# Performance work log

Hardware: AMD Instinct MI355X
Metric: run time of the kernel (lower is better)

Reference implementation:

```python
import jax, jax.numpy as jnp
import numpy as np
from jax import lax

V = 33      # n_vertices
EPS = 1e-5  # instance-norm eps


def _resize_bilinear(x, oh, ow):
    # torch F.interpolate bilinear, align_corners=False, antialias=False
    b, c, H, W = x.shape
    def coords(out, size):
        src = (jnp.arange(out, dtype=jnp.float32) + 0.5) * (size / out) - 0.5
        i0 = jnp.clip(jnp.floor(src).astype(jnp.int32), 0, size - 1)
        i1 = jnp.clip(i0 + 1, 0, size - 1)
        f = jnp.clip(src - i0.astype(jnp.float32), 0.0, 1.0)
        return i0, i1, f
    y0, y1, fy = coords(oh, H)
    x0, x1, fx = coords(ow, W)
    rows = x[:, :, y0, :] * (1 - fy)[None, None, :, None] + x[:, :, y1, :] * fy[None, None, :, None]
    return rows[:, :, :, x0] * (1 - fx) + rows[:, :, :, x1] * fx


def _conv_s2(x, w, b):
    y = lax.conv_general_dilated(x, w, (2, 2), [(1, 1), (1, 1)],
                                 dimension_numbers=('NCHW', 'OIHW', 'NCHW'))
    return y + b[None, :, None, None]


def _lrelu(x):
    return jnp.where(x >= 0, x, 0.2 * x)


def _inorm(x, g, be):
    m = x.mean((2, 3), keepdims=True)
    v = x.var((2, 3), keepdims=True)
    return (x - m) / jnp.sqrt(v + EPS) * g[None, :, None, None] + be[None, :, None, None]


def _ailut_transform(imgs, luts, vertices):
    # imgs (b,3,H,W); luts (b,3,V,V,V) indexed [out_c, ib, ig, ir]; vertices (b,3,V)
    b, c, H, W = imgs.shape
    N = H * W
    x = jnp.clip(imgs, 0.0, 1.0).reshape(b, 3, N)
    ss = jax.vmap(jax.vmap(lambda v, q: jnp.searchsorted(v, q, side='right')))
    idx = jnp.clip(ss(vertices, x) - 1, 0, V - 2)            # (b,3,N)
    v0 = jnp.take_along_axis(vertices, idx, axis=-1)
    v1 = jnp.take_along_axis(vertices, idx + 1, axis=-1)
    frac = jnp.clip((x - v0) / jnp.maximum(v1 - v0, 1e-10), 0.0, 1.0)
    ir, ig, ibl = idx[:, 0], idx[:, 1], idx[:, 2]            # (b,N) each
    fr, fg, fb = frac[:, 0], frac[:, 1], frac[:, 2]
    lut_flat = luts.reshape(b, 3, V * V * V)
    out = jnp.zeros((b, 3, N), imgs.dtype)
    for db in (0, 1):
        wb = fb if db else 1.0 - fb
        for dg in (0, 1):
            wg = fg if dg else 1.0 - fg
            for dr in (0, 1):
                w = wb * wg * (fr if dr else 1.0 - fr)       # (b,N)
                flat = ((ibl + db) * V + (ig + dg)) * V + (ir + dr)
                vals = jnp.take_along_axis(lut_flat, jnp.broadcast_to(flat[:, None, :], (b, 3, N)), axis=-1)
                out = out + w[:, None, :] * vals
    return out.reshape(b, 3, H, W)


def setup_inputs() -> dict:
    key = jax.random.key(0)
    ks = jax.random.split(key, 32)
    n = lambda k, s: jax.random.normal(k, s, jnp.float32) * 0.05
    inp = {'imgs': jax.random.uniform(ks[0], (2, 3, 2048, 2048), jnp.float32)}
    chans = [(3, 16), (16, 32), (32, 64), (64, 128), (128, 128)]
    for i, (ci, co) in enumerate(chans, start=1):
        inp[f'w{i}'] = n(ks[2 * i], (co, ci, 3, 3))
        inp[f'b{i}'] = n(ks[2 * i + 1], (co,))
        if i <= 4:
            inp[f'g{i}'] = jnp.ones((co,), jnp.float32)
            inp[f'be{i}'] = jnp.zeros((co,), jnp.float32)
    inp['wgen_w'] = n(ks[12], (512, 3))
    inp['wgen_b'] = n(ks[13], (3,))
    inp['basis_w'] = n(ks[14], (3, 3 * V ** 3))
    inp['ada_w'] = n(ks[15], (512, 3 * (V - 1)))
    inp['ada_b'] = n(ks[16], (3 * (V - 1),))
    return inp


def reference(imgs, w1, b1, g1, be1, w2, b2, g2, be2, w3, b3, g3, be3,
              w4, b4, g4, be4, w5, b5, wgen_w, wgen_b, basis_w, ada_w, ada_b):
    b = imgs.shape[0]
    x = _resize_bilinear(imgs, 256, 256)
    for (w, bb, g, be) in ((w1, b1, g1, be1), (w2, b2, g2, be2),
                           (w3, b3, g3, be3), (w4, b4, g4, be4)):
        x = _inorm(_lrelu(_conv_s2(x, w, bb)), g, be)
    x = _lrelu(_conv_s2(x, w5, b5))                      # (b,128,8,8); dropout is identity at eval
    x = x.reshape(b, 128, 2, 4, 2, 4).mean((3, 5)).reshape(b, 512)  # AdaptiveAvgPool2d(2)
    weights = x @ wgen_w + wgen_b                        # (b,3) rank weights
    luts = (weights @ basis_w).reshape(b, 3, V, V, V)
    intervals = jax.nn.softmax((x @ ada_w + ada_b).reshape(b, 3, V - 1), axis=-1)
    vertices = jnp.pad(jnp.cumsum(intervals, -1), ((0, 0), (0, 0), (1, 0)))  # (b,3,V)
    return _ailut_transform(imgs, luts, vertices)
```

## Files before the change

kernel.cpp:

```cpp
#include <hip/hip_runtime.h>
#include <hip/hip_fp16.h>
#include <cstdint>
#include <cstddef>

#define VCUBE 35937
#define LUT_CH 107811

typedef float fx4 __attribute__((ext_vector_type(4)));

__global__ __launch_bounds__(256) void conv1_fused(const float* __restrict__ imgs,
    const float* __restrict__ w, const float* __restrict__ bias,
    float* __restrict__ out) {
  __shared__ float s_in[3*3*34];
  __shared__ float s_w[16*3*9];
  int bid = blockIdx.x;
  int owt = bid & 7; int oh = (bid >> 3) & 127; int b = bid >> 10;
  int t = threadIdx.x;
  int ow0 = owt * 16;
  int iwbase = 2*ow0 - 1;
  int ihbase = 2*oh - 1;
  for (int i = t; i < 3*3*34; i += 256) {
    int x = i % 34; int rest = i / 34; int kh = rest % 3; int ci = rest / 3;
    int ih = ihbase + kh;
    int iw = iwbase + x;
    float v = 0.f;
    if (ih >= 0 && ih < 256 && iw >= 0 && iw < 256) {
      const float* p = imgs + (size_t)(b*3+ci) * 2048 * 2048;
      int y0 = ih*8 + 3, x0 = iw*8 + 3;
      const float* r0 = p + (size_t)y0*2048 + x0;
      const float* r1 = r0 + 2048;
      float a = r0[0], bb = r0[1], c = r1[0], d = r1[1];
      float top = a + 0.5f*(bb - a);
      float bot = c + 0.5f*(d - c);
      v = top + 0.5f*(bot - top);
    }
    s_in[i] = v;
  }
  for (int i = t; i < 16*3*9; i += 256) s_w[i] = w[i];
  __syncthreads();
  int owl = t & 15; int co = t >> 4;
  float acc = bias[co];
  const float* wp = s_w + co*27;
#pragma unroll
  for (int ci = 0; ci < 3; ci++) {
#pragma unroll
    for (int kh = 0; kh < 3; kh++) {
      const float* rp = s_in + (ci*3 + kh)*34 + 2*owl;
      acc = fmaf(rp[0], wp[ci*9 + kh*3 + 0], acc);
      acc = fmaf(rp[1], wp[ci*9 + kh*3 + 1], acc);
      acc = fmaf(rp[2], wp[ci*9 + kh*3 + 2], acc);
    }
  }
  acc = acc >= 0.f ? acc : 0.2f*acc;
  out[(((size_t)b*16 + co)*128 + oh)*128 + ow0 + owl] = acc;
}

template<int CI, int CO, int IS, int COPB, bool WLDS>
__global__ __launch_bounds__(256) void conv_row(const float* __restrict__ in,
    const float* __restrict__ w, const float* __restrict__ bias,
    float* __restrict__ out) {
  constexpr int OS = IS/2;
  constexpr int PW = IS + 2;
  constexpr int NG = CO/COPB;
  constexpr int E  = CI*3*PW;
  static_assert(COPB*OS == 256, "block mismatch");
  __shared__ float s_in[E];
  __shared__ float s_w[WLDS ? COPB*CI*9 : 1];
  int bid = blockIdx.x;
  int grp = bid % NG; int rest = bid / NG; int oh = rest % OS; int b = rest / OS;
  int t = threadIdx.x;
  int ihb = 2*oh - 1;
  for (int i = t; i < E; i += 256) {
    int x = i % PW; int r2 = i / PW; int kh = r2 % 3; int ci = r2 / 3;
    int ih = ihb + kh; int iw = x - 1;
    float v = 0.f;
    if (ih >= 0 && ih < IS && iw >= 0 && iw < IS)
      v = in[((size_t)(b*CI + ci)*IS + ih)*IS + iw];
    s_in[i] = v;
  }
  if (WLDS) {
    const float* wg = w + (size_t)grp*COPB*CI*9;
    for (int i = t; i < COPB*CI*9; i += 256) s_w[i] = wg[i];
  }
  __syncthreads();
  int ow = t % OS; int col = t / OS;
  int co = grp*COPB + col;
  float acc = bias[co];
  const float* wp = WLDS ? (s_w + col*CI*9) : (w + (size_t)co*CI*9);
  for (int ci = 0; ci < CI; ci++) {
    const float* rowp = s_in + ci*3*PW;
    const float* wc = wp + ci*9;
#pragma unroll
    for (int kh = 0; kh < 3; kh++) {
      const float* rp = rowp + kh*PW + 2*ow;
      acc = fmaf(rp[0], wc[kh*3 + 0], acc);
      acc = fmaf(rp[1], wc[kh*3 + 1], acc);
      acc = fmaf(rp[2], wc[kh*3 + 2], acc);
    }
  }
  acc = acc >= 0.f ? acc : 0.2f*acc;
  out[(((size_t)b*CO + co)*OS + oh)*OS + ow] = acc;
}

__global__ __launch_bounds__(256) void inorm_kernel(float* __restrict__ x,
    const float* __restrict__ g, const float* __restrict__ be, int C, int HW) {
  int plane = blockIdx.x;
  int c = plane % C;
  float* p = x + (size_t)plane * HW;
  int t = threadIdx.x;
  float s = 0.f, s2 = 0.f;
  for (int i = t; i < HW; i += 256) {
    float v = p[i];
    s += v;
    s2 = fmaf(v, v, s2);
  }
  __shared__ float ss[256], sq[256];
  ss[t] = s; sq[t] = s2;
  __syncthreads();
  for (int off = 128; off > 0; off >>= 1) {
    if (t < off) { ss[t] += ss[t + off]; sq[t] += sq[t + off]; }
    __syncthreads();
  }
  __shared__ float sc, sh;
  if (t == 0) {
    float inv_n = 1.0f / (float)HW;
    float mean = ss[0] * inv_n;
    float var  = sq[0] * inv_n - mean*mean;
    float scale = g[c] / sqrtf(var + 1e-5f);
    sc = scale;
    sh = be[c] - mean*scale;
  }
  __syncthreads();
  for (int i = t; i < HW; i += 256) p[i] = fmaf(p[i], sc, sh);
}

__global__ __launch_bounds__(128) void head_kernel(const float* __restrict__ x5,
    const float* __restrict__ wgen_w, const float* __restrict__ wgen_b,
    const float* __restrict__ ada_w, const float* __restrict__ ada_b,
    float* __restrict__ gweights, float* __restrict__ vertices,
    float* __restrict__ invtab, uint8_t* __restrict__ hints) {
  int b = blockIdx.x; int t = threadIdx.x;
  __shared__ float xv[512];
  __shared__ float logits[96];
  __shared__ float svp[99];
  for (int o = t; o < 512; o += 128) {
    int c = o >> 2; int h2 = (o >> 1) & 1; int w2 = o & 1;
    const float* p = x5 + ((size_t)(b*128 + c))*64 + h2*32 + w2*4;
    float s = 0.f;
#pragma unroll
    for (int h = 0; h < 4; h++)
#pragma unroll
      for (int ww = 0; ww < 4; ww++) s += p[h*8 + ww];
    xv[o] = s * (1.f/16.f);
  }
  __syncthreads();
  if (t < 96) {
    float s = ada_b[t];
    for (int k = 0; k < 512; k++) s = fmaf(xv[k], ada_w[k*96 + t], s);
    logits[t] = s;
  } else if (t < 99) {
    int j = t - 96;
    float s = wgen_b[j];
    for (int k = 0; k < 512; k++) s = fmaf(xv[k], wgen_w[k*3 + j], s);
    gweights[b*3 + j] = s;
  }
  __syncthreads();
  if (t < 3) {
    const float* l = logits + t*32;
    float m = l[0];
#pragma unroll
    for (int i = 1; i < 32; i++) m = fmaxf(m, l[i]);
    float e[32]; float sum = 0.f;
#pragma unroll
    for (int i = 0; i < 32; i++) { e[i] = expf(l[i] - m); sum += e[i]; }
    float inv = 1.0f / sum;
    float* vp = vertices + b*99 + t*33;
    svp[t*33] = 0.f; vp[0] = 0.f;
    float cum = 0.f;
#pragma unroll
    for (int i = 0; i < 32; i++) { cum = fmaf(e[i], inv, cum); svp[t*33 + i + 1] = cum; vp[i + 1] = cum; }
  }
  __syncthreads();
  if (t < 96) {
    int c = t >> 5, i = t & 31;
    float d = svp[c*33 + i + 1] - svp[c*33 + i];
    invtab[b*96 + t] = 1.0f / fmaxf(d, 1e-10f);
  }
  for (int e = t; e < 3072; e += 128) {
    int c = e >> 10; int bin = e & 1023;
    float q0 = (float)bin * (1.f/1024.f);
    const float* v = svp + c*33;
    int lo = 0, hi = 33;
    while (lo < hi) { int mid = (lo + hi) >> 1; if (v[mid] <= q0) lo = mid + 1; else hi = mid; }
    int idx = lo - 1; if (idx > 31) idx = 31;
    hints[b*3072 + e] = (uint8_t)idx;
  }
}

__global__ __launch_bounds__(256) void ecell_build(const float* __restrict__ basis_w,
    const float* __restrict__ gw, __half* __restrict__ ecell, int B) {
  int tid = blockIdx.x*256 + threadIdx.x;
  int total = B * 32768 * 3;
  if (tid >= total) return;
  int cc = tid % 3;
  int cell = tid / 3;
  int r = cell & 31; int g = (cell >> 5) & 31; int bl = (cell >> 10) & 31; int b = cell >> 15;
  float w0 = gw[b*3 + 0], w1 = gw[b*3 + 1], w2 = gw[b*3 + 2];
  union { __half h[8]; uint4 u; } pk;
#pragma unroll
  for (int dbl = 0; dbl < 2; dbl++)
#pragma unroll
    for (int dg = 0; dg < 2; dg++)
#pragma unroll
      for (int dr = 0; dr < 2; dr++) {
        int flat = cc*VCUBE + ((bl + dbl)*33 + (g + dg))*33 + (r + dr);
        float val = w0*basis_w[flat] + w1*basis_w[LUT_CH + flat] + w2*basis_w[2*LUT_CH + flat];
        pk.h[dbl*4 + dg*2 + dr] = __float2half(val);
      }
  *(uint4*)((uint16_t*)ecell + (size_t)cell*32 + cc*8) = pk.u;
}

__device__ __forceinline__ float trilerp_cell(uint4 u, float fR, float fG, float fB) {
  const __half* h = (const __half*)&u;
  float f0 = __half2float(h[0]), f1 = __half2float(h[1]);
  float f2 = __half2float(h[2]), f3 = __half2float(h[3]);
  float f4 = __half2float(h[4]), f5 = __half2float(h[5]);
  float f6 = __half2float(h[6]), f7 = __half2float(h[7]);
  float l00 = fmaf(fR, f1 - f0, f0);
  float l01 = fmaf(fR, f3 - f2, f2);
  float L0  = fmaf(fG, l01 - l00, l00);
  float l10 = fmaf(fR, f5 - f4, f4);
  float l11 = fmaf(fR, f7 - f6, f6);
  float L1  = fmaf(fG, l11 - l10, l10);
  return fmaf(fB, L1 - L0, L0);
}

__global__ __launch_bounds__(256, 4) void transform_kernel(const float* __restrict__ imgs,
    const __half* __restrict__ ecell, const float* __restrict__ vert,
    const float* __restrict__ invtab, const unsigned int* __restrict__ hintw,
    float* __restrict__ out, int B) {
  const size_t N = 2048u*2048u;
  __shared__ float sv[112];
  __shared__ unsigned int shint_w[768];
  int b = blockIdx.x % B;
  int pblk = blockIdx.x / B;
  int t = threadIdx.x;
  if (t < 108) {
    int c = t / 36, i = t - c*36;
    sv[t] = (i < 33) ? vert[b*99 + c*33 + i] : 2.0f;
  }
  for (int i = t; i < 768; i += 256) shint_w[i] = hintw[b*768 + i];
  __syncthreads();
  const uint8_t* shint = (const uint8_t*)shint_w;
  size_t pix = ((size_t)pblk*256 + t) * 4;
  const float* ip = imgs + (size_t)b*3*N;
  float* op = out + (size_t)b*3*N;
  const __half* ec = ecell + (size_t)b*1048576;

  fx4 r  = __builtin_nontemporal_load((const fx4*)(ip + pix));
  fx4 g  = __builtin_nontemporal_load((const fx4*)(ip + N + pix));
  fx4 bb = __builtin_nontemporal_load((const fx4*)(ip + 2*N + pix));

  float qv[3][4] = { { r.x, r.y, r.z, r.w },
                     { g.x, g.y, g.z, g.w },
                     { bb.x, bb.y, bb.z, bb.w } };
  int   idxv[3][4];
  float frv[3][4];

#pragma unroll
  for (int c = 0; c < 3; c++) {
#pragma unroll
    for (int p = 0; p < 4; p++) {
      float qc = fminf(fmaxf(qv[c][p], 0.f), 1.f);
      int bin = (int)(qc * 1024.f); bin = bin > 1023 ? 1023 : bin;
      int h = shint[(c << 10) + bin];
      const float* vv = sv + c*36 + h;
      float v0 = vv[0], v1 = vv[1], v2 = vv[2], v3 = vv[3], v4 = vv[4];
      int cnt = (int)(v1 <= qc) + (int)(v2 <= qc) + (int)(v3 <= qc);
      int cmax = 31 - h; cnt = cnt < cmax ? cnt : cmax;
      float lo = v0, hi = v1;
      lo = cnt >= 1 ? v1 : lo;  hi = cnt >= 1 ? v2 : hi;
      lo = cnt >= 2 ? v2 : lo;  hi = cnt >= 2 ? v3 : hi;
      lo = cnt >= 3 ? v3 : lo;  hi = cnt >= 3 ? v4 : hi;
      idxv[c][p] = h + cnt;
      float f = (qc - lo) * __builtin_amdgcn_rcpf(fmaxf(hi - lo, 1e-10f));
      frv[c][p] = fminf(fmaxf(f, 0.f), 1.f);
    }
  }

  uint4 u0[4], u1[4], u2[4];
#pragma unroll
  for (int p = 0; p < 4; p++) {
    const __half* cell = ec +
        ((size_t)(((idxv[2][p] << 5) + idxv[1][p]) << 5) + idxv[0][p]) * 32;
    u0[p] = *(const uint4*)(cell);
    u1[p] = *(const uint4*)(cell + 8);
    u2[p] = *(const uint4*)(cell + 16);
  }

  fx4 o0, o1, o2;
#pragma unroll
  for (int p = 0; p < 4; p++) {
    float fR = frv[0][p], fG = frv[1][p], fB = frv[2][p];
    float a0 = trilerp_cell(u0[p], fR, fG, fB);
    float a1 = trilerp_cell(u1[p], fR, fG, fB);
    float a2 = trilerp_cell(u2[p], fR, fG, fB);
    if (p == 0) { o0.x = a0; o1.x = a1; o2.x = a2; }
    if (p == 1) { o0.y = a0; o1.y = a1; o2.y = a2; }
    if (p == 2) { o0.z = a0; o1.z = a1; o2.z = a2; }
    if (p == 3) { o0.w = a0; o1.w = a1; o2.w = a2; }
  }
  __builtin_nontemporal_store(o0, (fx4*)(op + pix));
  __builtin_nontemporal_store(o1, (fx4*)(op + N + pix));
  __builtin_nontemporal_store(o2, (fx4*)(op + 2*N + pix));
}

extern "C" void kernel_launch(void* const* d_in, const int* in_sizes, int n_in,
                              void* d_out, int out_size, void* d_ws, size_t ws_size,
                              hipStream_t stream) {
  const float* imgs = (const float*)d_in[0];
  const float* w1 = (const float*)d_in[1];  const float* b1 = (const float*)d_in[2];
  const float* g1 = (const float*)d_in[3];  const float* be1 = (const float*)d_in[4];
  const float* w2 = (const float*)d_in[5];  const float* b2 = (const float*)d_in[6];
  const float* g2 = (const float*)d_in[7];  const float* be2 = (const float*)d_in[8];
  const float* w3 = (const float*)d_in[9];  const float* b3 = (const float*)d_in[10];
  const float* g3 = (const float*)d_in[11]; const float* be3 = (const float*)d_in[12];
  const float* w4 = (const float*)d_in[13]; const float* b4 = (const float*)d_in[14];
  const float* g4 = (const float*)d_in[15]; const float* be4 = (const float*)d_in[16];
  const float* w5 = (const float*)d_in[17]; const float* b5 = (const float*)d_in[18];
  const float* wgen_w  = (const float*)d_in[19];
  const float* wgen_b  = (const float*)d_in[20];
  const float* basis_w = (const float*)d_in[21];
  const float* ada_w   = (const float*)d_in[22];
  const float* ada_b   = (const float*)d_in[23];
  float* out = (float*)d_out;

  const int B = in_sizes[0] / (3*2048*2048);

  char* wsb = (char*)d_ws;
  __half* ecell = (__half*)wsb;
  size_t A_bytes = (size_t)B * 2097152;
  float* x1 = (float*)wsb;
  float* x2 = x1 + (size_t)B*262144;
  float* x3 = x2 + (size_t)B*131072;
  float* x4 = x3 + (size_t)B*65536;
  float* x5 = x4 + (size_t)B*32768;
  float* tail = (float*)(wsb + A_bytes);
  float* gw   = tail;
  float* vert = gw + (size_t)B*4;
  float* invt = vert + (size_t)B*99;
  uint8_t* hints = (uint8_t*)(invt + (size_t)B*96);

  conv1_fused<<<B*1024, 256, 0, stream>>>(imgs, w1, b1, x1);
  inorm_kernel<<<B*16, 256, 0, stream>>>(x1, g1, be1, 16, 128*128);
  conv_row<16, 32, 128, 4, true><<<B*512, 256, 0, stream>>>(x1, w2, b2, x2);
  inorm_kernel<<<B*32, 256, 0, stream>>>(x2, g2, be2, 32, 64*64);
  conv_row<32, 64, 64, 8, true><<<B*256, 256, 0, stream>>>(x2, w3, b3, x3);
  inorm_kernel<<<B*64, 256, 0, stream>>>(x3, g3, be3, 64, 32*32);
  conv_row<64, 128, 32, 16, true><<<B*128, 256, 0, stream>>>(x3, w4, b4, x4);
  inorm_kernel<<<B*128, 256, 0, stream>>>(x4, g4, be4, 128, 16*16);
  conv_row<128, 128, 16, 32, false><<<B*32, 256, 0, stream>>>(x4, w5, b5, x5);
  head_kernel<<<B, 128, 0, stream>>>(x5, wgen_w, wgen_b, ada_w, ada_b, gw, vert, invt, hints);
  ecell_build<<<B*384, 256, 0, stream>>>(basis_w, gw, ecell, B);
  transform_kernel<<<B*4096, 256, 0, stream>>>(imgs, ecell, vert, invt,
                                               (const unsigned int*)hints, out, B);
}
```

Before: 453.9 us.

## Stage per-pixel LUT metadata in shared memory and remap lanes to channels

The transform kernel now computes each pixel's cell index and fractions, writes them to shared memory, and after a barrier reassigns work so four adjacent lanes cover one pixel, three of them each fetching one channel's 16-byte LUT slice. Neighbouring lanes therefore read contiguous 48 bytes of a cell instead of one thread issuing three loads. Output becomes scalar nontemporal stores, coalesced across lanes, in place of per-thread float4 stores. In exchange it adds a 16KB shared buffer and a barrier, idles a quarter of lanes in the gather phase, and uses narrower stores, all of which can lower occupancy and throughput.

After: 473.6 us. 1.04x slower.

```diff
diff --git a/kernel.cpp b/kernel.cpp
--- a/kernel.cpp
+++ b/kernel.cpp
@@ -242,6 +242,7 @@
   const size_t N = 2048u*2048u;
   __shared__ float sv[112];
   __shared__ unsigned int shint_w[768];
+  __shared__ uint4 s_meta[1024];
   int b = blockIdx.x % B;
   int pblk = blockIdx.x / B;
   int t = threadIdx.x;
@@ -252,7 +253,8 @@
   for (int i = t; i < 768; i += 256) shint_w[i] = hintw[b*768 + i];
   __syncthreads();
   const uint8_t* shint = (const uint8_t*)shint_w;
-  size_t pix = ((size_t)pblk*256 + t) * 4;
+  size_t base = (size_t)pblk * 1024;
+  size_t pix = base + (size_t)t * 4;
   const float* ip = imgs + (size_t)b*3*N;
   float* op = out + (size_t)b*3*N;
   const __half* ec = ecell + (size_t)b*1048576;
@@ -264,13 +266,12 @@
   float qv[3][4] = { { r.x, r.y, r.z, r.w },
                      { g.x, g.y, g.z, g.w },
                      { bb.x, bb.y, bb.z, bb.w } };
-  int   idxv[3][4];
-  float frv[3][4];
-
-#pragma unroll
-  for (int c = 0; c < 3; c++) {
-#pragma unroll
-    for (int p = 0; p < 4; p++) {
+
+#pragma unroll
+  for (int p = 0; p < 4; p++) {
+    int idxc[3]; float frc[3];
+#pragma unroll
+    for (int c = 0; c < 3; c++) {
       float qc = fminf(fmaxf(qv[c][p], 0.f), 1.f);
       int bin = (int)(qc * 1024.f); bin = bin > 1023 ? 1023 : bin;
       int h = shint[(c << 10) + bin];
@@ -282,37 +283,33 @@
       lo = cnt >= 1 ? v1 : lo;  hi = cnt >= 1 ? v2 : hi;
       lo = cnt >= 2 ? v2 : lo;  hi = cnt >= 2 ? v3 : hi;
       lo = cnt >= 3 ? v3 : lo;  hi = cnt >= 3 ? v4 : hi;
-      idxv[c][p] = h + cnt;
+      idxc[c] = h + cnt;
       float f = (qc - lo) * __builtin_amdgcn_rcpf(fmaxf(hi - lo, 1e-10f));
-      frv[c][p] = fminf(fmaxf(f, 0.f), 1.f);
-    }
-  }
-
-  uint4 u0[4], u1[4], u2[4];
-#pragma unroll
-  for (int p = 0; p < 4; p++) {
-    const __half* cell = ec +
-        ((size_t)(((idxv[2][p] << 5) + idxv[1][p]) << 5) + idxv[0][p]) * 32;
-    u0[p] = *(const uint4*)(cell);
-    u1[p] = *(const uint4*)(cell + 8);
-    u2[p] = *(const uint4*)(cell + 16);
-  }
-
-  fx4 o0, o1, o2;
-#pragma unroll
-  for (int p = 0; p < 4; p++) {
-    float fR = frv[0][p], fG = frv[1][p], fB = frv[2][p];
-    float a0 = trilerp_cell(u0[p], fR, fG, fB);
-    float a1 = trilerp_cell(u1[p], fR, fG, fB);
-    float a2 = trilerp_cell(u2[p], fR, fG, fB);
-    if (p == 0) { o0.x = a0; o1.x = a1; o2.x = a2; }
-    if (p == 1) { o0.y = a0; o1.y = a1; o2.y = a2; }
-    if (p == 2) { o0.z = a0; o1.z = a1; o2.z = a2; }
-    if (p == 3) { o0.w = a0; o1.w = a1; o2.w = a2; }
-  }
-  __builtin_nontemporal_store(o0, (fx4*)(op + pix));
-  __builtin_nontemporal_store(o1, (fx4*)(op + N + pix));
-  __builtin_nontemporal_store(o2, (fx4*)(op + 2*N + pix));
+      frc[c] = fminf(fmaxf(f, 0.f), 1.f);
+    }
+    uint4 m;
+    m.x = (unsigned)((((idxc[2] << 5) + idxc[1]) << 5) + idxc[0]);
+    m.y = __float_as_uint(frc[0]);
+    m.z = __float_as_uint(frc[1]);
+    m.w = __float_as_uint(frc[2]);
+    s_meta[p*256 + t] = m;
+  }
+  __syncthreads();
+
+  int c   = t & 3;
+  int sub = t >> 2;
+#pragma unroll 4
+  for (int j = 0; j < 16; j++) {
+    int q = j*64 + sub;
+    uint4 m = s_meta[(q & 3)*256 + (q >> 2)];
+    if (c < 3) {
+      const uint16_t* cell = (const uint16_t*)ec + (size_t)m.x * 32;
+      uint4 u = *(const uint4*)(cell + c*8);
+      float res = trilerp_cell(u, __uint_as_float(m.y), __uint_as_float(m.z),
+                               __uint_as_float(m.w));
+      __builtin_nontemporal_store(res, op + (size_t)c*N + base + (size_t)q);
+    }
+  }
 }
 
 extern "C" void kernel_launch(void* const* d_in, const int* in_sizes, int n_in,
```

## Merge CNN and LUT-build stages into one cooperative persistent kernel

Applied to the files above, without the earlier changes.

Replaces the eleven separate launches (conv1, four inorms, four conv_row, head, ecell_build) with a single cooperative kernel of 256 blocks. Each stage loops over its virtual blocks and is separated from the next by grid.sync, using one shared scratch buffer in LDS. It also drops the unused inverse-interval table from the head stage and from the transform kernel's arguments. The goal is to remove per-launch overhead and the idle gaps between small kernels. The cost is a fixed grid with one large LDS allocation per block, so it runs at low occupancy and gives up latency hiding in the heavier conv stages.

After: 777.4 us. +71.3%, slower.

```diff
diff --git a/kernel.cpp b/kernel.cpp
--- a/kernel.cpp
+++ b/kernel.cpp
@@ -1,21 +1,23 @@
 #include <hip/hip_runtime.h>
 #include <hip/hip_fp16.h>
+#include <hip/hip_cooperative_groups.h>
 #include <cstdint>
 #include <cstddef>
 
+namespace cg = cooperative_groups;
+
 #define VCUBE 35937
 #define LUT_CH 107811
 
 typedef float fx4 __attribute__((ext_vector_type(4)));
 
-__global__ __launch_bounds__(256) void conv1_fused(const float* __restrict__ imgs,
-    const float* __restrict__ w, const float* __restrict__ bias,
-    float* __restrict__ out) {
-  __shared__ float s_in[3*3*34];
-  __shared__ float s_w[16*3*9];
-  int bid = blockIdx.x;
+
+__device__ __forceinline__ void conv1_body(int bid, int t,
+    const float* __restrict__ imgs, const float* __restrict__ w,
+    const float* __restrict__ bias, float* __restrict__ out, float* smem) {
+  float* s_in = smem;
+  float* s_w  = smem + 320;
   int owt = bid & 7; int oh = (bid >> 3) & 127; int b = bid >> 10;
-  int t = threadIdx.x;
   int ow0 = owt * 16;
   int iwbase = 2*ow0 - 1;
   int ihbase = 2*oh - 1;
@@ -53,22 +55,21 @@
   }
   acc = acc >= 0.f ? acc : 0.2f*acc;
   out[(((size_t)b*16 + co)*128 + oh)*128 + ow0 + owl] = acc;
+  __syncthreads();
 }
 
 template<int CI, int CO, int IS, int COPB, bool WLDS>
-__global__ __launch_bounds__(256) void conv_row(const float* __restrict__ in,
-    const float* __restrict__ w, const float* __restrict__ bias,
-    float* __restrict__ out) {
+__device__ __forceinline__ void conv_row_body(int bid, int t,
+    const float* __restrict__ in, const float* __restrict__ w,
+    const float* __restrict__ bias, float* __restrict__ out, float* smem) {
   constexpr int OS = IS/2;
   constexpr int PW = IS + 2;
   constexpr int NG = CO/COPB;
   constexpr int E  = CI*3*PW;
   static_assert(COPB*OS == 256, "block mismatch");
-  __shared__ float s_in[E];
-  __shared__ float s_w[WLDS ? COPB*CI*9 : 1];
-  int bid = blockIdx.x;
+  float* s_in = smem;
+  float* s_w  = smem + E;
   int grp = bid % NG; int rest = bid / NG; int oh = rest % OS; int b = rest / OS;
-  int t = threadIdx.x;
   int ihb = 2*oh - 1;
   for (int i = t; i < E; i += 256) {
     int x = i % PW; int r2 = i / PW; int kh = r2 % 3; int ci = r2 / 3;
@@ -100,50 +101,51 @@
   }
   acc = acc >= 0.f ? acc : 0.2f*acc;
   out[(((size_t)b*CO + co)*OS + oh)*OS + ow] = acc;
-}
-
-__global__ __launch_bounds__(256) void inorm_kernel(float* __restrict__ x,
-    const float* __restrict__ g, const float* __restrict__ be, int C, int HW) {
-  int plane = blockIdx.x;
+  __syncthreads();
+}
+
+__device__ __forceinline__ void inorm_body(int plane, int t, float* __restrict__ x,
+    const float* __restrict__ g, const float* __restrict__ be, int C, int HW,
+    float* smem) {
   int c = plane % C;
   float* p = x + (size_t)plane * HW;
-  int t = threadIdx.x;
   float s = 0.f, s2 = 0.f;
   for (int i = t; i < HW; i += 256) {
     float v = p[i];
     s += v;
     s2 = fmaf(v, v, s2);
   }
-  __shared__ float ss[256], sq[256];
+  float* ss = smem; float* sq = smem + 256;
   ss[t] = s; sq[t] = s2;
   __syncthreads();
   for (int off = 128; off > 0; off >>= 1) {
     if (t < off) { ss[t] += ss[t + off]; sq[t] += sq[t + off]; }
     __syncthreads();
   }
-  __shared__ float sc, sh;
   if (t == 0) {
     float inv_n = 1.0f / (float)HW;
     float mean = ss[0] * inv_n;
     float var  = sq[0] * inv_n - mean*mean;
     float scale = g[c] / sqrtf(var + 1e-5f);
-    sc = scale;
-    sh = be[c] - mean*scale;
-  }
-  __syncthreads();
+    smem[512] = scale;
+    smem[513] = be[c] - mean*scale;
+  }
+  __syncthreads();
+  float sc = smem[512], sh = smem[513];
   for (int i = t; i < HW; i += 256) p[i] = fmaf(p[i], sc, sh);
-}
-
-__global__ __launch_bounds__(128) void head_kernel(const float* __restrict__ x5,
+  __syncthreads();
+}
+
+__device__ __forceinline__ void head_body(int b, int t,
+    const float* __restrict__ x5,
     const float* __restrict__ wgen_w, const float* __restrict__ wgen_b,
     const float* __restrict__ ada_w, const float* __restrict__ ada_b,
     float* __restrict__ gweights, float* __restrict__ vertices,
-    float* __restrict__ invtab, uint8_t* __restrict__ hints) {
-  int b = blockIdx.x; int t = threadIdx.x;
-  __shared__ float xv[512];
-  __shared__ float logits[96];
-  __shared__ float svp[99];
-  for (int o = t; o < 512; o += 128) {
+    uint8_t* __restrict__ hints, float* smem) {
+  float* xv = smem;
+  float* logits = smem + 512;
+  float* svp = smem + 608;
+  for (int o = t; o < 512; o += 256) {
     int c = o >> 2; int h2 = (o >> 1) & 1; int w2 = o & 1;
     const float* p = x5 + ((size_t)(b*128 + c))*64 + h2*32 + w2*4;
     float s = 0.f;
@@ -181,12 +183,7 @@
     for (int i = 0; i < 32; i++) { cum = fmaf(e[i], inv, cum); svp[t*33 + i + 1] = cum; vp[i + 1] = cum; }
   }
   __syncthreads();
-  if (t < 96) {
-    int c = t >> 5, i = t & 31;
-    float d = svp[c*33 + i + 1] - svp[c*33 + i];
-    invtab[b*96 + t] = 1.0f / fmaxf(d, 1e-10f);
-  }
-  for (int e = t; e < 3072; e += 128) {
+  for (int e = t; e < 3072; e += 256) {
     int c = e >> 10; int bin = e & 1023;
     float q0 = (float)bin * (1.f/1024.f);
     const float* v = svp + c*33;
@@ -195,11 +192,13 @@
     int idx = lo - 1; if (idx > 31) idx = 31;
     hints[b*3072 + e] = (uint8_t)idx;
   }
-}
-
-__global__ __launch_bounds__(256) void ecell_build(const float* __restrict__ basis_w,
-    const float* __restrict__ gw, __half* __restrict__ ecell, int B) {
-  int tid = blockIdx.x*256 + threadIdx.x;
+  __syncthreads();
+}
+
+__device__ __forceinline__ void ecell_body(int vb, int t,
+    const float* __restrict__ basis_w, const float* __restrict__ gw,
+    __half* __restrict__ ecell, int B) {
+  int tid = vb*256 + t;
   int total = B * 32768 * 3;
   if (tid >= total) return;
   int cc = tid % 3;
@@ -218,6 +217,63 @@
         pk.h[dbl*4 + dg*2 + dr] = __float2half(val);
       }
   *(uint4*)((uint16_t*)ecell + (size_t)cell*32 + cc*8) = pk.u;
+}
+
+__global__ __launch_bounds__(256) void cnn_mega(
+    const float* __restrict__ imgs,
+    const float* __restrict__ w1, const float* __restrict__ b1,
+    const float* __restrict__ g1, const float* __restrict__ be1,
+    const float* __restrict__ w2, const float* __restrict__ b2,
+    const float* __restrict__ g2, const float* __restrict__ be2,
+    const float* __restrict__ w3, const float* __restrict__ b3,
+    const float* __restrict__ g3, const float* __restrict__ be3,
+    const float* __restrict__ w4, const float* __restrict__ b4,
+    const float* __restrict__ g4, const float* __restrict__ be4,
+    const float* __restrict__ w5, const float* __restrict__ b5,
+    const float* __restrict__ wgen_w, const float* __restrict__ wgen_b,
+    const float* __restrict__ basis_w,
+    const float* __restrict__ ada_w, const float* __restrict__ ada_b,
+    float* __restrict__ x1, float* __restrict__ x2, float* __restrict__ x3,
+    float* __restrict__ x4, float* __restrict__ x5,
+    float* __restrict__ gw, float* __restrict__ vert, uint8_t* __restrict__ hints,
+    __half* __restrict__ ecell, int B) {
+  cg::grid_group grid = cg::this_grid();
+  __shared__ float smem[16384];
+  int t = threadIdx.x;
+  int nb = gridDim.x;
+
+  for (int vb = blockIdx.x; vb < B*1024; vb += nb)
+    conv1_body(vb, t, imgs, w1, b1, x1, smem);
+  grid.sync();
+  for (int vb = blockIdx.x; vb < B*16; vb += nb)
+    inorm_body(vb, t, x1, g1, be1, 16, 128*128, smem);
+  grid.sync();
+  for (int vb = blockIdx.x; vb < B*512; vb += nb)
+    conv_row_body<16, 32, 128, 4, true>(vb, t, x1, w2, b2, x2, smem);
+  grid.sync();
+  for (int vb = blockIdx.x; vb < B*32; vb += nb)
+    inorm_body(vb, t, x2, g2, be2, 32, 64*64, smem);
+  grid.sync();
+  for (int vb = blockIdx.x; vb < B*256; vb += nb)
+    conv_row_body<32, 64, 64, 8, true>(vb, t, x2, w3, b3, x3, smem);
+  grid.sync();
+  for (int vb = blockIdx.x; vb < B*64; vb += nb)
+    inorm_body(vb, t, x3, g3, be3, 64, 32*32, smem);
+  grid.sync();
+  for (int vb = blockIdx.x; vb < B*128; vb += nb)
+    conv_row_body<64, 128, 32, 16, true>(vb, t, x3, w4, b4, x4, smem);
+  grid.sync();
+  for (int vb = blockIdx.x; vb < B*128; vb += nb)
+    inorm_body(vb, t, x4, g4, be4, 128, 16*16, smem);
+  grid.sync();
+  for (int vb = blockIdx.x; vb < B*32; vb += nb)
+    conv_row_body<128, 128, 16, 32, false>(vb, t, x4, w5, b5, x5, smem);
+  grid.sync();
+  for (int vb = blockIdx.x; vb < B; vb += nb)
+    head_body(vb, t, x5, wgen_w, wgen_b, ada_w, ada_b, gw, vert, hints, smem);
+  grid.sync();
+  for (int vb = blockIdx.x; vb < B*384; vb += nb)
+    ecell_body(vb, t, basis_w, gw, ecell, B);
 }
 
 __device__ __forceinline__ float trilerp_cell(uint4 u, float fR, float fG, float fB) {
@@ -237,7 +293,7 @@
 
 __global__ __launch_bounds__(256, 4) void transform_kernel(const float* __restrict__ imgs,
     const __half* __restrict__ ecell, const float* __restrict__ vert,
-    const float* __restrict__ invtab, const unsigned int* __restrict__ hintw,
+    const unsigned int* __restrict__ hintw,
     float* __restrict__ out, int B) {
   const size_t N = 2048u*2048u;
   __shared__ float sv[112];
@@ -348,20 +404,23 @@
   float* tail = (float*)(wsb + A_bytes);
   float* gw   = tail;
   float* vert = gw + (size_t)B*4;
-  float* invt = vert + (size_t)B*99;
-  uint8_t* hints = (uint8_t*)(invt + (size_t)B*96);
-
-  conv1_fused<<<B*1024, 256, 0, stream>>>(imgs, w1, b1, x1);
-  inorm_kernel<<<B*16, 256, 0, stream>>>(x1, g1, be1, 16, 128*128);
-  conv_row<16, 32, 128, 4, true><<<B*512, 256, 0, stream>>>(x1, w2, b2, x2);
-  inorm_kernel<<<B*32, 256, 0, stream>>>(x2, g2, be2, 32, 64*64);
-  conv_row<32, 64, 64, 8, true><<<B*256, 256, 0, stream>>>(x2, w3, b3, x3);
-  inorm_kernel<<<B*64, 256, 0, stream>>>(x3, g3, be3, 64, 32*32);
-  conv_row<64, 128, 32, 16, true><<<B*128, 256, 0, stream>>>(x3, w4, b4, x4);
-  inorm_kernel<<<B*128, 256, 0, stream>>>(x4, g4, be4, 128, 16*16);
-  conv_row<128, 128, 16, 32, false><<<B*32, 256, 0, stream>>>(x4, w5, b5, x5);
-  head_kernel<<<B, 128, 0, stream>>>(x5, wgen_w, wgen_b, ada_w, ada_b, gw, vert, invt, hints);
-  ecell_build<<<B*384, 256, 0, stream>>>(basis_w, gw, ecell, B);
-  transform_kernel<<<B*4096, 256, 0, stream>>>(imgs, ecell, vert, invt,
+  uint8_t* hints = (uint8_t*)(vert + (size_t)B*99);
+
+  int Bc = B;
+  void* margs[] = {
+    (void*)&imgs,
+    (void*)&w1, (void*)&b1, (void*)&g1, (void*)&be1,
+    (void*)&w2, (void*)&b2, (void*)&g2, (void*)&be2,
+    (void*)&w3, (void*)&b3, (void*)&g3, (void*)&be3,
+    (void*)&w4, (void*)&b4, (void*)&g4, (void*)&be4,
+    (void*)&w5, (void*)&b5,
+    (void*)&wgen_w, (void*)&wgen_b, (void*)&basis_w, (void*)&ada_w, (void*)&ada_b,
+    (void*)&x1, (void*)&x2, (void*)&x3, (void*)&x4, (void*)&x5,
+    (void*)&gw, (void*)&vert, (void*)&hints, (void*)&ecell, (void*)&Bc
+  };
+  hipLaunchCooperativeKernel((const void*)cnn_mega, dim3(256), dim3(256),
+                             margs, 0, stream);
+
+  transform_kernel<<<B*4096, 256, 0, stream>>>(imgs, ecell, vert,
                                                (const unsigned int*)hints, out, B);
 }
```
